# Kernel tuning notes

Measured on AMD Instinct MI355X. Metric: run time of the kernel, lower is better.

Reference implementation:

```python
import jax, jax.numpy as jnp
import numpy as np
import math

B, S, HID, H = 2, 1024, 512, 8
D = HID // H  # 64
EPS = 1e-24


def setup_inputs() -> dict:
    key = jax.random.key(0)
    ks = jax.random.split(key, 12)
    s = 0.02
    return {
        "input_tensor": jax.random.normal(ks[0], (B, S, HID), dtype=jnp.float32),
        "attention_mask": jnp.zeros((B, 1, S, S), dtype=jnp.float32),
        # Linear weights stored as [in, out] (y = x @ W + b)
        "Wq": jax.random.normal(ks[1], (HID, HID), dtype=jnp.float32) * s,
        "bq": jnp.zeros((HID,), dtype=jnp.float32),
        "Wk": jax.random.normal(ks[2], (HID, HID), dtype=jnp.float32) * s,
        "bk": jnp.zeros((HID,), dtype=jnp.float32),
        "Wv": jax.random.normal(ks[3], (HID, HID), dtype=jnp.float32) * s,
        "bv": jnp.zeros((HID,), dtype=jnp.float32),
        # order_affine: Linear(2*D, 1)
        "order_w": jax.random.normal(ks[4], (2 * D,), dtype=jnp.float32) * s,
        "order_b": jnp.zeros((), dtype=jnp.float32),
        # distance_affine: Linear(2*D, 1)
        "dist_w": jax.random.normal(ks[5], (2 * D,), dtype=jnp.float32) * s,
        "dist_b": jnp.zeros((), dtype=jnp.float32),
        "scalar": jax.random.normal(ks[6], (1,), dtype=jnp.float32),
    }


def _heads(x):  # [B,S,HID] -> [B,H,S,D]
    return x.reshape(B, S, H, D).transpose(0, 2, 1, 3)


def reference(input_tensor, attention_mask, Wq, bq, Wk, bk, Wv, bv,
              order_w, order_b, dist_w, dist_b, scalar):
    scale = math.sqrt(D)

    mixed_q = input_tensor @ Wq + bq            # [B,S,HID]
    mixed_k = input_tensor @ Wk + bk
    mixed_v = input_tensor @ Wv + bv

    qh = _heads(mixed_q)                        # [B,H,S,D]
    kh = _heads(mixed_k)
    vh = _heads(mixed_v)

    scores = jnp.einsum('bhid,bhjd->bhij', qh, kh)   # [B,H,S,S]
    origin_scores = scores

    # --- order bias: sigmoid(affine(cat(q_i, k_j))) decomposed (same math,
    # avoids materializing the [B,H,S,S,2D] concat the torch code builds) ---
    q_ord = jnp.einsum('bhid,d->bhi', qh, order_w[:D])    # [B,H,S]
    k_ord = jnp.einsum('bhjd,d->bhj', kh, order_w[D:])
    pr_order = jax.nn.sigmoid(q_ord[..., :, None] + k_ord[..., None, :] + order_b)
    gd_order = jnp.triu(jnp.ones((S, S), dtype=scores.dtype), k=1)  # 1 where j>i
    error_order = (jnp.log(pr_order + EPS) * gd_order
                   + jnp.log(1.0 - pr_order + EPS) * (1.0 - gd_order))

    # --- distance bias ---
    idx = jnp.arange(S)
    gd_distance = jnp.log(jnp.abs(idx[None, :] - idx[:, None]).astype(scores.dtype) + 1.0)
    q_dst = jnp.einsum('bhid,d->bhi', qh, dist_w[:D])
    k_dst = jnp.einsum('bhjd,d->bhj', kh, dist_w[D:])
    pr_distance = q_dst[..., :, None] + k_dst[..., None, :] + dist_b   # [B,H,S,S]
    error_distance = -jnp.square(gd_distance - pr_distance) * jnp.square(scalar[0]) * 0.5

    adj_scores = scores + error_order + error_distance

    def _probs(sc):
        return jax.nn.softmax(sc / scale + attention_mask, axis=-1)

    attention_probs = _probs(adj_scores)
    origin_attention_probs = _probs(origin_scores)

    return (mixed_q, mixed_k, vh, attention_probs, origin_attention_probs)
```

## Files before the change

### kernel.cpp

```cpp
#include <hip/hip_runtime.h>
#include <math.h>

#define Sdim 1024
#define HIDdim 512
#define Hnum 8
#define Ddim 64

typedef __attribute__((ext_vector_type(4))) float f32x4;
typedef __attribute__((ext_vector_type(8))) short short8;
typedef __attribute__((ext_vector_type(4))) unsigned short ushort4v;

static __device__ __forceinline__ unsigned short f2bf(float x) {
    union { float f; unsigned u; } v; v.f = x;
    unsigned r = v.u + 0x7fffu + ((v.u >> 16) & 1u);
    return (unsigned short)(r >> 16);
}

__global__ __launch_bounds__(256) void qkv_gemm(
    const float* __restrict__ X,
    const float* __restrict__ Wq, const float* __restrict__ bq,
    const float* __restrict__ Wk, const float* __restrict__ bk,
    const float* __restrict__ Wv, const float* __restrict__ bv,
    float* __restrict__ outq, float* __restrict__ outk, float* __restrict__ outv)
{
    __shared__ unsigned short Ws[64][72];
    __shared__ unsigned short Xs[64][72];

    const int mb = blockIdx.x;
    const int nb = blockIdx.y;
    const int which = nb >> 3;
    const int n0 = (nb & 7) * 64;
    const float* __restrict__ W    = (which == 0) ? Wq : (which == 1) ? Wk : Wv;
    const float* __restrict__ bias = (which == 0) ? bq : (which == 1) ? bk : bv;

    const int t    = threadIdx.x;
    const int lane = t & 63;
    const int w    = t >> 6;
    const int g    = lane >> 4;
    const int c    = lane & 15;
    const int m0r  = mb * 64;

    f32x4 acc[4];
#pragma unroll
    for (int f = 0; f < 4; ++f) { f32x4 z = {0.f, 0.f, 0.f, 0.f}; acc[f] = z; }

    for (int kt = 0; kt < 512; kt += 64) {
        __syncthreads();
        {
            const int row = t >> 2, kb = (t & 3) * 16;
            const float* __restrict__ src = &X[(size_t)(m0r + row) * HIDdim + kt + kb];
#pragma unroll
            for (int i = 0; i < 4; ++i) {
                const f32x4 v = *(const f32x4*)&src[4 * i];
                ushort4v p;
                p.x = f2bf(v.x); p.y = f2bf(v.y); p.z = f2bf(v.z); p.w = f2bf(v.w);
                *(ushort4v*)&Xs[row][kb + 4 * i] = p;
            }
        }
#pragma unroll
        for (int p = 0; p < 4; ++p) {
            const int kr   = p * 16 + (t >> 4);
            const int nloc = (t & 15) * 4;
            const f32x4 v = *(const f32x4*)&W[(size_t)(kt + kr) * HIDdim + n0 + nloc];
            Ws[nloc + 0][kr] = f2bf(v.x);
            Ws[nloc + 1][kr] = f2bf(v.y);
            Ws[nloc + 2][kr] = f2bf(v.z);
            Ws[nloc + 3][kr] = f2bf(v.w);
        }
        __syncthreads();
        const short8 a0 = *(const short8*)&Ws[w * 16 + c][g * 8];
        const short8 a1 = *(const short8*)&Ws[w * 16 + c][32 + g * 8];
#pragma unroll
        for (int f = 0; f < 4; ++f) {
            const short8 b0 = *(const short8*)&Xs[f * 16 + c][g * 8];
            const short8 b1 = *(const short8*)&Xs[f * 16 + c][32 + g * 8];
            acc[f] = __builtin_amdgcn_mfma_f32_16x16x32_bf16(a0, b0, acc[f], 0, 0, 0);
            acc[f] = __builtin_amdgcn_mfma_f32_16x16x32_bf16(a1, b1, acc[f], 0, 0, 0);
        }
    }

    const int nql = w * 16 + g * 4;
    const f32x4 bb = *(const f32x4*)&bias[n0 + nql];
#pragma unroll
    for (int f = 0; f < 4; ++f) {
        const int m = m0r + f * 16 + c;
        f32x4 v = acc[f] + bb;
        if (which == 2) {
            const int b = m >> 10, s = m & 1023;
            const int h = nb & 7;
            *(f32x4*)&outv[((((size_t)b * Hnum + h) * Sdim) + s) * Ddim + nql] = v;
        } else {
            float* __restrict__ o = (which == 0) ? outq : outk;
            *(f32x4*)&o[(size_t)m * HIDdim + n0 + nql] = v;
        }
    }
}

__global__ __launch_bounds__(256) void prep_kernel(
    const float* __restrict__ mq, const float* __restrict__ mk,
    const float* __restrict__ order_w, const float* __restrict__ dist_w,
    unsigned short* __restrict__ qbf, unsigned short* __restrict__ kbf,
    float* __restrict__ qog, float* __restrict__ qdg,
    float* __restrict__ kog, float* __restrict__ kdg)
{
    const int tg  = blockIdx.x * 256 + threadIdx.x;
    const int row = tg >> 3;
    const int dc8 = (tg & 7) * 8;
    const int bh  = row >> 10, s = row & 1023;
    const int b   = bh >> 3,   h = bh & 7;
    const size_t src = ((size_t)b * Sdim + s) * HIDdim + h * Ddim + dc8;

    const f32x4 ow0 = *(const f32x4*)&order_w[dc8];
    const f32x4 ow1 = *(const f32x4*)&order_w[dc8 + 4];
    const f32x4 dw0 = *(const f32x4*)&dist_w[dc8];
    const f32x4 dw1 = *(const f32x4*)&dist_w[dc8 + 4];
    const f32x4 owk0 = *(const f32x4*)&order_w[Ddim + dc8];
    const f32x4 owk1 = *(const f32x4*)&order_w[Ddim + dc8 + 4];
    const f32x4 dwk0 = *(const f32x4*)&dist_w[Ddim + dc8];
    const f32x4 dwk1 = *(const f32x4*)&dist_w[Ddim + dc8 + 4];

    {
        const f32x4 v0 = *(const f32x4*)&mq[src];
        const f32x4 v1 = *(const f32x4*)&mq[src + 4];
        float po = v0.x * ow0.x + v0.y * ow0.y + v0.z * ow0.z + v0.w * ow0.w
                 + v1.x * ow1.x + v1.y * ow1.y + v1.z * ow1.z + v1.w * ow1.w;
        float pd = v0.x * dw0.x + v0.y * dw0.y + v0.z * dw0.z + v0.w * dw0.w
                 + v1.x * dw1.x + v1.y * dw1.y + v1.z * dw1.z + v1.w * dw1.w;
#pragma unroll
        for (int o = 1; o < 8; o <<= 1) { po += __shfl_xor(po, o); pd += __shfl_xor(pd, o); }
        if ((tg & 7) == 0) { qog[row] = po; qdg[row] = pd; }
        ushort4v p0, p1;
        p0.x = f2bf(v0.x); p0.y = f2bf(v0.y); p0.z = f2bf(v0.z); p0.w = f2bf(v0.w);
        p1.x = f2bf(v1.x); p1.y = f2bf(v1.y); p1.z = f2bf(v1.z); p1.w = f2bf(v1.w);
        *(ushort4v*)&qbf[(size_t)row * Ddim + dc8]     = p0;
        *(ushort4v*)&qbf[(size_t)row * Ddim + dc8 + 4] = p1;
    }
    {
        const f32x4 v0 = *(const f32x4*)&mk[src];
        const f32x4 v1 = *(const f32x4*)&mk[src + 4];
        float po = v0.x * owk0.x + v0.y * owk0.y + v0.z * owk0.z + v0.w * owk0.w
                 + v1.x * owk1.x + v1.y * owk1.y + v1.z * owk1.z + v1.w * owk1.w;
        float pd = v0.x * dwk0.x + v0.y * dwk0.y + v0.z * dwk0.z + v0.w * dwk0.w
                 + v1.x * dwk1.x + v1.y * dwk1.y + v1.z * dwk1.z + v1.w * dwk1.w;
#pragma unroll
        for (int o = 1; o < 8; o <<= 1) { po += __shfl_xor(po, o); pd += __shfl_xor(pd, o); }
        if ((tg & 7) == 0) { kog[row] = po; kdg[row] = pd; }
        ushort4v p0, p1;
        p0.x = f2bf(v0.x); p0.y = f2bf(v0.y); p0.z = f2bf(v0.z); p0.w = f2bf(v0.w);
        p1.x = f2bf(v1.x); p1.y = f2bf(v1.y); p1.z = f2bf(v1.z); p1.w = f2bf(v1.w);
        *(ushort4v*)&kbf[(size_t)row * Ddim + dc8]     = p0;
        *(ushort4v*)&kbf[(size_t)row * Ddim + dc8 + 4] = p1;
    }
}

__global__ __launch_bounds__(512, 4) void attn_kernel(
    const unsigned short* __restrict__ qbf, const unsigned short* __restrict__ kbf,
    const float* __restrict__ qog, const float* __restrict__ qdg,
    const float* __restrict__ kog, const float* __restrict__ kdg,
    const float* __restrict__ mask,
    const float* __restrict__ order_b_p, const float* __restrict__ dist_b_p,
    const float* __restrict__ scalar_p,
    float* __restrict__ out_adj, float* __restrict__ out_orig)
{
    __shared__ float gdl[Sdim];
    __shared__ float red_s[16][8];

    const int t    = threadIdx.x;
    const int lane = t & 63;
    const int w    = t >> 6;
    const int g    = lane >> 4;
    const int c    = lane & 15;

    const int blk = blockIdx.x;
    const int ib  = blk & 63;
    const int bh  = blk >> 6;
    const int b   = bh >> 3;
    const int i0  = ib * 16;
    const int i   = i0 + c;

    const float order_b = order_b_p[0];
    const float dist_b  = dist_b_p[0];
    const float sc      = scalar_p[0];
    const float sc2h    = 0.5f * sc * sc;
    const float mscale  = 0.125f;

    {
        const int idx = t * 2;
        gdl[idx]     = __logf((float)idx + 1.0f);
        gdl[idx + 1] = __logf((float)idx + 2.0f);
    }
    __syncthreads();

    const size_t hbase = (size_t)bh * Sdim;
    const size_t qrow = (hbase + i) * Ddim;
    const short8 qf0 = *(const short8*)&qbf[qrow + g * 8];
    const short8 qf1 = *(const short8*)&qbf[qrow + 32 + g * 8];

    f32x4 acc[8];
#pragma unroll
    for (int it = 0; it < 8; ++it) { f32x4 z = {0.f, 0.f, 0.f, 0.f}; acc[it] = z; }

#pragma unroll
    for (int it = 0; it < 8; ++it) {
        const size_t kr = (hbase + it * 128 + w * 16 + c) * Ddim;
        const short8 kf0 = *(const short8*)&kbf[kr + g * 8];
        const short8 kf1 = *(const short8*)&kbf[kr + 32 + g * 8];
        acc[it] = __builtin_amdgcn_mfma_f32_16x16x32_bf16(kf0, qf0, acc[it], 0, 0, 0);
        acc[it] = __builtin_amdgcn_mfma_f32_16x16x32_bf16(kf1, qf1, acc[it], 0, 0, 0);
    }

    const size_t obase = (size_t)bh * Sdim * Sdim;
    const float* __restrict__ mrow = &mask[((size_t)b * Sdim + i) * Sdim];

    float s0 = 0.0f;
#pragma unroll
    for (int it = 0; it < 8; ++it) {
        const int j0 = it * 128 + w * 16 + g * 4;
        const f32x4 mk4 = *(const f32x4*)&mrow[j0];
        f32x4 l = acc[it] * mscale + mk4;
        acc[it] = l;
        s0 += __expf(l[0]) + __expf(l[1]) + __expf(l[2]) + __expf(l[3]);
    }
    s0 += __shfl_xor(s0, 16);
    s0 += __shfl_xor(s0, 32);
    if (lane < 16) red_s[lane][w] = s0;
    __syncthreads();
    f32x4 ra = *(const f32x4*)&red_s[c][0];
    f32x4 rb = *(const f32x4*)&red_s[c][4];
    const float inv0 = __builtin_amdgcn_rcpf(ra[0] + ra[1] + ra[2] + ra[3]
                                           + rb[0] + rb[1] + rb[2] + rb[3]);
    {
        float* __restrict__ orow = out_orig + obase + (size_t)i * Sdim;
#pragma unroll
        for (int it = 0; it < 8; ++it) {
            const int j0 = it * 128 + w * 16 + g * 4;
            const f32x4 l = acc[it];
            f32x4 p;
            p[0] = __expf(l[0]) * inv0; p[1] = __expf(l[1]) * inv0;
            p[2] = __expf(l[2]) * inv0; p[3] = __expf(l[3]) * inv0;
            *(f32x4*)&orow[j0] = p;
        }
    }

    const float qo = qog[hbase + i] + order_b;
    const float qd = qdg[hbase + i] + dist_b;
    float s1 = 0.0f;
#pragma unroll
    for (int it = 0; it < 8; ++it) {
        const int j0 = it * 128 + w * 16 + g * 4;
        const f32x4 ko4 = *(const f32x4*)&kog[hbase + j0];
        const f32x4 kd4 = *(const f32x4*)&kdg[hbase + j0];
        f32x4 l = acc[it];
#pragma unroll
        for (int r = 0; r < 4; ++r) {
            const int j = j0 + r;
            const float z    = qo + ko4[r];
            const float targ = (j > i) ? -z : z;
            const float pe   = -__logf(1.0f + __expf(targ));
            const int   dl   = (i > j) ? (i - j) : (j - i);
            const float df   = gdl[dl] - (qd + kd4[r]);
            l[r] += (pe - sc2h * df * df) * mscale;
            s1 += __expf(l[r]);
        }
        acc[it] = l;
    }
    __syncthreads();
    s1 += __shfl_xor(s1, 16);
    s1 += __shfl_xor(s1, 32);
    if (lane < 16) red_s[lane][w] = s1;
    __syncthreads();
    ra = *(const f32x4*)&red_s[c][0];
    rb = *(const f32x4*)&red_s[c][4];
    const float inv1 = __builtin_amdgcn_rcpf(ra[0] + ra[1] + ra[2] + ra[3]
                                           + rb[0] + rb[1] + rb[2] + rb[3]);
    {
        float* __restrict__ arow = out_adj + obase + (size_t)i * Sdim;
#pragma unroll
        for (int it = 0; it < 8; ++it) {
            const int j0 = it * 128 + w * 16 + g * 4;
            const f32x4 l = acc[it];
            f32x4 p;
            p[0] = __expf(l[0]) * inv1; p[1] = __expf(l[1]) * inv1;
            p[2] = __expf(l[2]) * inv1; p[3] = __expf(l[3]) * inv1;
            *(f32x4*)&arow[j0] = p;
        }
    }
}

extern "C" void kernel_launch(void* const* d_in, const int* in_sizes, int n_in,
                              void* d_out, int out_size, void* d_ws, size_t ws_size,
                              hipStream_t stream) {
    const float* X    = (const float*)d_in[0];
    const float* mask = (const float*)d_in[1];
    const float* Wq   = (const float*)d_in[2];
    const float* bq   = (const float*)d_in[3];
    const float* Wk   = (const float*)d_in[4];
    const float* bk   = (const float*)d_in[5];
    const float* Wv   = (const float*)d_in[6];
    const float* bv   = (const float*)d_in[7];
    const float* ow   = (const float*)d_in[8];
    const float* ob   = (const float*)d_in[9];
    const float* dw   = (const float*)d_in[10];
    const float* db   = (const float*)d_in[11];
    const float* sc   = (const float*)d_in[12];

    float* out     = (float*)d_out;
    float* outq    = out;
    float* outk    = out + 1048576;
    float* outv    = out + 2097152;
    float* outadj  = out + 3145728;
    float* outorig = out + 19922944;

    unsigned short* qbf = (unsigned short*)d_ws;
    unsigned short* kbf = qbf + 16384 * 64;
    float* qog = (float*)(kbf + 16384 * 64);
    float* qdg = qog + 16384;
    float* kog = qdg + 16384;
    float* kdg = kog + 16384;

    qkv_gemm<<<dim3(32, 24), 256, 0, stream>>>(X, Wq, bq, Wk, bk, Wv, bv,
                                               outq, outk, outv);
    prep_kernel<<<dim3(512), 256, 0, stream>>>(outq, outk, ow, dw,
                                               qbf, kbf, qog, qdg, kog, kdg);
    attn_kernel<<<dim3(1024), 512, 0, stream>>>(qbf, kbf, qog, qdg, kog, kdg,
                                                mask, ob, db, sc,
                                                outadj, outorig);
}
```

Baseline: 83.03 us.

## Stage softmax outputs through LDS for coalesced row stores and cut exp count

Softmax probabilities are written to a shared-memory tile and then stored by each wave as contiguous full rows, replacing scattered 16-column fragments per row. Exponentials are computed once and reused: the original logits are kept as exp values, and the adjusted softmax multiplies them by an exp of the bias term instead of recomputing exp of the sum. The large LDS tile (about 66KB) reduces how many blocks can be resident per CU and adds barriers.

After: 79.64 us. -4.1%, faster.

```diff
diff --git a/kernel.cpp b/kernel.cpp
--- a/kernel.cpp
+++ b/kernel.cpp
@@ -162,6 +162,7 @@
     const float* __restrict__ scalar_p,
     float* __restrict__ out_adj, float* __restrict__ out_orig)
 {
+    __shared__ float ps[16][1036];
     __shared__ float gdl[Sdim];
     __shared__ float red_s[16][8];
 
@@ -192,7 +193,7 @@
     __syncthreads();
 
     const size_t hbase = (size_t)bh * Sdim;
-    const size_t qrow = (hbase + i) * Ddim;
+    const size_t qrow  = (hbase + i) * Ddim;
     const short8 qf0 = *(const short8*)&qbf[qrow + g * 8];
     const short8 qf1 = *(const short8*)&qbf[qrow + 32 + g * 8];
 
@@ -217,9 +218,11 @@
     for (int it = 0; it < 8; ++it) {
         const int j0 = it * 128 + w * 16 + g * 4;
         const f32x4 mk4 = *(const f32x4*)&mrow[j0];
-        f32x4 l = acc[it] * mscale + mk4;
-        acc[it] = l;
-        s0 += __expf(l[0]) + __expf(l[1]) + __expf(l[2]) + __expf(l[3]);
+        f32x4 e;
+#pragma unroll
+        for (int r = 0; r < 4; ++r) e[r] = __expf(fmaf(acc[it][r], mscale, mk4[r]));
+        acc[it] = e;
+        s0 += e[0] + e[1] + e[2] + e[3];
     }
     s0 += __shfl_xor(s0, 16);
     s0 += __shfl_xor(s0, 32);
@@ -229,16 +232,22 @@
     f32x4 rb = *(const f32x4*)&red_s[c][4];
     const float inv0 = __builtin_amdgcn_rcpf(ra[0] + ra[1] + ra[2] + ra[3]
                                            + rb[0] + rb[1] + rb[2] + rb[3]);
-    {
-        float* __restrict__ orow = out_orig + obase + (size_t)i * Sdim;
-#pragma unroll
-        for (int it = 0; it < 8; ++it) {
-            const int j0 = it * 128 + w * 16 + g * 4;
-            const f32x4 l = acc[it];
-            f32x4 p;
-            p[0] = __expf(l[0]) * inv0; p[1] = __expf(l[1]) * inv0;
-            p[2] = __expf(l[2]) * inv0; p[3] = __expf(l[3]) * inv0;
-            *(f32x4*)&orow[j0] = p;
+
+#pragma unroll
+    for (int it = 0; it < 8; ++it) {
+        const int colw = it * 128 + w * 16 + g * 4;
+        f32x4 p = acc[it] * inv0;
+        *(f32x4*)&ps[c][colw] = p;
+    }
+    __syncthreads();
+    {
+        float* __restrict__ obuf = out_orig + obase + (size_t)i0 * Sdim;
+#pragma unroll
+        for (int n = 0; n < 8; ++n) {
+            const int row = 2 * w + (n >> 2);
+            const int col = (n & 3) * 256 + lane * 4;
+            const f32x4 v = *(const f32x4*)&ps[row][col];
+            *(f32x4*)&obuf[(size_t)row * Sdim + col] = v;
         }
     }
 
@@ -250,21 +259,21 @@
         const int j0 = it * 128 + w * 16 + g * 4;
         const f32x4 ko4 = *(const f32x4*)&kog[hbase + j0];
         const f32x4 kd4 = *(const f32x4*)&kdg[hbase + j0];
-        f32x4 l = acc[it];
+        f32x4 p = acc[it];
 #pragma unroll
         for (int r = 0; r < 4; ++r) {
             const int j = j0 + r;
             const float z    = qo + ko4[r];
             const float targ = (j > i) ? -z : z;
-            const float pe   = -__logf(1.0f + __expf(targ));
+            const float u    = 1.0f + __expf(targ);
             const int   dl   = (i > j) ? (i - j) : (j - i);
             const float df   = gdl[dl] - (qd + kd4[r]);
-            l[r] += (pe - sc2h * df * df) * mscale;
-            s1 += __expf(l[r]);
-        }
-        acc[it] = l;
-    }
-    __syncthreads();
+            const float eD   = __expf(-0.125f * fmaf(sc2h * df, df, __logf(u)));
+            p[r] *= eD;
+            s1 += p[r];
+        }
+        acc[it] = p;
+    }
     s1 += __shfl_xor(s1, 16);
     s1 += __shfl_xor(s1, 32);
     if (lane < 16) red_s[lane][w] = s1;
@@ -273,16 +282,22 @@
     rb = *(const f32x4*)&red_s[c][4];
     const float inv1 = __builtin_amdgcn_rcpf(ra[0] + ra[1] + ra[2] + ra[3]
                                            + rb[0] + rb[1] + rb[2] + rb[3]);
-    {
-        float* __restrict__ arow = out_adj + obase + (size_t)i * Sdim;
-#pragma unroll
-        for (int it = 0; it < 8; ++it) {
-            const int j0 = it * 128 + w * 16 + g * 4;
-            const f32x4 l = acc[it];
-            f32x4 p;
-            p[0] = __expf(l[0]) * inv1; p[1] = __expf(l[1]) * inv1;
-            p[2] = __expf(l[2]) * inv1; p[3] = __expf(l[3]) * inv1;
-            *(f32x4*)&arow[j0] = p;
+
+#pragma unroll
+    for (int it = 0; it < 8; ++it) {
+        const int colw = it * 128 + w * 16 + g * 4;
+        f32x4 p = acc[it] * inv1;
+        *(f32x4*)&ps[c][colw] = p;
+    }
+    __syncthreads();
+    {
+        float* __restrict__ abuf = out_adj + obase + (size_t)i0 * Sdim;
+#pragma unroll
+        for (int n = 0; n < 8; ++n) {
+            const int row = 2 * w + (n >> 2);
+            const int col = (n & 3) * 256 + lane * 4;
+            const f32x4 v = *(const f32x4*)&ps[row][col];
+            *(f32x4*)&abuf[(size_t)row * Sdim + col] = v;
         }
     }
 }
```
